# Kernel tuning notes

Measured on AMD Instinct MI355X. Metric: run time of the kernel, lower is better.

Reference implementation:

```python
import jax, jax.numpy as jnp
import numpy as np

N_PREV = 65536
BATCH = 2048
DIM = 128


def setup_inputs() -> dict:
    key = jax.random.key(0)
    k1, k2 = jax.random.split(key)
    n = N_PREV + BATCH
    target_lib = jax.random.normal(k1, (n, DIM), dtype=jnp.float32)
    reached_lib = jax.random.normal(k2, (n, DIM), dtype=jnp.float32)
    return {
        "target_goal_embedding_library": target_lib,
        "reached_goal_embedding_library": reached_lib,
        "batch_size": BATCH,
    }


def reference(target_goal_embedding_library, reached_goal_embedding_library, batch_size):
    # slice the library: last batch_size rows are current target/reached goals
    tg = target_goal_embedding_library[-batch_size:]      # [B, D]
    rg = reached_goal_embedding_library[-batch_size:]     # [B, D]
    prev = reached_goal_embedding_library[:-batch_size]   # [N_prev, D]

    # brute-force squared euclidean distances via gram trick: [B, N_prev]
    d2 = (
        jnp.sum(tg * tg, axis=-1, keepdims=True)
        - 2.0 * tg @ prev.T
        + jnp.sum(prev * prev, axis=-1)[None, :]
    )
    idx = jnp.argmin(d2, axis=1)          # top-1 nearest neighbor ids, [B]
    closest = prev[idx]                   # [B, D] gather

    # LP(g, s, r) = ||g - s|| - ||g - r||; value and grad wrt g, vmapped over batch
    def LP(g, s, r):
        return (
            jnp.sqrt(jnp.sum(jnp.square(g - s), axis=-1))
            - jnp.sqrt(jnp.sum(jnp.square(g - r), axis=-1))
        )

    IM_vals, IM_grads = jax.vmap(jax.value_and_grad(LP, 0), in_axes=(0, 0, 0))(
        tg, closest, rg
    )
    return IM_vals, IM_grads
```

## Files before the change

### kernel.cpp

```cpp
#include <hip/hip_runtime.h>
#include <math.h>

#define DIM 128
#define BATCH 2048
#define NPREV 65536
#define NCH 32
#define NJT 16
#define DELTA 0.4f

typedef __attribute__((ext_vector_type(8))) short bf16x8;
typedef __attribute__((ext_vector_type(4))) float f32x4;
typedef unsigned short u16;

static __device__ __forceinline__ unsigned short f2bf(float f) {
    unsigned int u = __float_as_uint(f);
    u += 0x7FFF + ((u >> 16) & 1);
    return (unsigned short)(u >> 16);
}

#define GLOAD16(g, l) __builtin_amdgcn_global_load_lds( \
    (const __attribute__((address_space(1))) void*)(g), \
    (__attribute__((address_space(3))) void*)(l), 16, 0, 0)

__global__ __launch_bounds__(256) void k_convB(const float* __restrict__ src,
                                               u16* __restrict__ dst,
                                               float* __restrict__ p2part) {
    int id = blockIdx.x * 256 + threadIdx.x;
    int img = id >> 10, c = id & 1023;
    int ks2 = c >> 9, rem = c & 511, row = rem >> 2, slot = rem & 3;
    int koct = slot ^ ((row >> 1) & 3);
    int srow = (img >> 1) * 128 + row;
    int scol = (img & 1) * 64 + ks2 * 32 + koct * 8;
    const float* s = src + (size_t)srow * DIM + scol;
    float4 f0 = *reinterpret_cast<const float4*>(s);
    float4 f1 = *reinterpret_cast<const float4*>(s + 4);
    float f[8] = {f0.x, f0.y, f0.z, f0.w, f1.x, f1.y, f1.z, f1.w};
    union { unsigned short us[8]; uint4 v; } o;
    float sum = 0.f;
    #pragma unroll
    for (int e = 0; e < 8; ++e) { o.us[e] = f2bf(f[e]); sum += f[e] * f[e]; }
    *reinterpret_cast<uint4*>(dst + (size_t)id * 8) = o.v;
    p2part[srow * 16 + (scol >> 3)] = sum;
}

__global__ __launch_bounds__(256) void k_prev2r(const float* __restrict__ p2part,
                                                float* __restrict__ prev2) {
    int row = blockIdx.x * 256 + threadIdx.x;
    const float4* p = reinterpret_cast<const float4*>(p2part + (size_t)row * 16);
    float4 a = p[0], b = p[1], c = p[2], d = p[3];
    float s = ((a.x + a.y) + (a.z + a.w)) + ((b.x + b.y) + (b.z + b.w))
            + ((c.x + c.y) + (c.z + c.w)) + ((d.x + d.y) + (d.z + d.w));
    prev2[row] = s;
}

__global__ __launch_bounds__(256) void k_convA(const float* __restrict__ src,
                                               u16* __restrict__ dst) {
    int id = blockIdx.x * 256 + threadIdx.x;
    int img = id >> 11, c = id & 2047;
    int ks2 = c >> 10, rem = c & 1023, row = rem >> 2, koct = rem & 3;
    int srow = (img >> 1) * 256 + row;
    int scol = (img & 1) * 64 + ks2 * 32 + koct * 8;
    const float* s = src + (size_t)srow * DIM + scol;
    float4 f0 = *reinterpret_cast<const float4*>(s);
    float4 f1 = *reinterpret_cast<const float4*>(s + 4);
    float f[8] = {f0.x, f0.y, f0.z, f0.w, f1.x, f1.y, f1.z, f1.w};
    union { unsigned short us[8]; uint4 v; } o;
    #pragma unroll
    for (int e = 0; e < 8; ++e) o.us[e] = f2bf(f[e]);
    *reinterpret_cast<uint4*>(dst + (size_t)id * 8) = o.v;
}

__global__ __launch_bounds__(512, 2) void k_gemm_argmin(
    const u16* __restrict__ Aimg, const u16* __restrict__ Bimg,
    const float* __restrict__ prev2, float4* __restrict__ partial)
{
    __shared__ __align__(16) u16 Bt[2][16384];

    const int t = threadIdx.x;
    const int lane = t & 63;
    const int w = t >> 6;
    const int l15 = lane & 15;
    const int lhi = lane >> 4;

    const int bid = blockIdx.x;
    const int mtile = bid >> 5;
    const int chunk = (bid & 7) + ((bid >> 3) & 3) * 8;

    const u16* gb0 = Bimg + (size_t)chunk * NJT * 16384;

    #pragma unroll
    for (int c = 0; c < 4; ++c)
        GLOAD16(gb0 + c * 4096 + t * 8, &Bt[0][c * 4096 + t * 8]);

    bf16x8 areg[2][2][2];
    {
        const u16* ab = Aimg + (size_t)mtile * 2 * 16384;
        #pragma unroll
        for (int kt = 0; kt < 2; ++kt)
            #pragma unroll
            for (int ks2 = 0; ks2 < 2; ++ks2)
                #pragma unroll
                for (int fm = 0; fm < 2; ++fm) {
                    int row = w * 32 + fm * 16 + l15;
                    areg[kt][ks2][fm] = *reinterpret_cast<const bf16x8*>(
                        ab + (size_t)kt * 16384 + (ks2 * 1024 + row * 4 + lhi) * 8);
                }
    }

    const int bbase = l15 * 64 + ((lhi ^ ((l15 >> 1) & 3)) << 4);
    const f32x4 z4 = {0.f, 0.f, 0.f, 0.f};

    float v1[2][4], v2[2][4]; int j1_[2][4], j2_[2][4];
    #pragma unroll
    for (int fm = 0; fm < 2; ++fm)
        #pragma unroll
        for (int r = 0; r < 4; ++r) {
            v1[fm][r] = INFINITY; v2[fm][r] = INFINITY;
            j1_[fm][r] = 0x7fffffff; j2_[fm][r] = 0x7fffffff;
        }

    for (int jt = 0; jt < NJT; ++jt) {
        const int p = jt & 1;
        __syncthreads();
        if (jt + 1 < NJT) {
            const u16* gb = gb0 + (size_t)(jt + 1) * 16384;
            u16* lb = Bt[p ^ 1];
            #pragma unroll
            for (int c = 0; c < 4; ++c)
                GLOAD16(gb + c * 4096 + t * 8, lb + c * 4096 + t * 8);
        }
        float p2f[8];
        #pragma unroll
        for (int fn = 0; fn < 8; ++fn)
            p2f[fn] = prev2[chunk * 2048 + jt * 128 + fn * 16 + l15];

        f32x4 acc[2][8];
        const char* Bc = (const char*)Bt[p];
        #pragma unroll
        for (int s = 0; s < 4; ++s) {
            const int img = s >> 1, ks2 = s & 1;
            bf16x8 bf[8];
            #pragma unroll
            for (int fn = 0; fn < 8; ++fn)
                bf[fn] = *reinterpret_cast<const bf16x8*>(
                    Bc + img * 16384 + ks2 * 8192 + fn * 1024 + bbase);
            if (s == 0) {
                #pragma unroll
                for (int fm = 0; fm < 2; ++fm)
                    #pragma unroll
                    for (int fn = 0; fn < 8; ++fn)
                        acc[fm][fn] = __builtin_amdgcn_mfma_f32_16x16x32_bf16(
                            areg[0][0][fm], bf[fn], z4, 0, 0, 0);
            } else {
                #pragma unroll
                for (int fm = 0; fm < 2; ++fm)
                    #pragma unroll
                    for (int fn = 0; fn < 8; ++fn)
                        acc[fm][fn] = __builtin_amdgcn_mfma_f32_16x16x32_bf16(
                            areg[img][ks2][fm], bf[fn], acc[fm][fn], 0, 0, 0);
            }
        }

        const int jb = chunk * 2048 + jt * 128 + l15;
        #pragma unroll
        for (int fm = 0; fm < 2; ++fm) {
            #pragma unroll
            for (int r = 0; r < 4; ++r) {
                float dmin = p2f[0] - 2.f * acc[fm][0][r]; int fs = 0;
                #pragma unroll
                for (int fn = 1; fn < 8; ++fn) {
                    float d = p2f[fn] - 2.f * acc[fm][fn][r];
                    if (d < dmin) { dmin = d; fs = fn; }
                }
                const int j = jb + fs * 16;
                const bool c1 = dmin < v1[fm][r];
                const bool c2 = dmin < v2[fm][r];
                v2[fm][r] = c1 ? v1[fm][r] : (c2 ? dmin : v2[fm][r]);
                j2_[fm][r] = c1 ? j1_[fm][r] : (c2 ? j    : j2_[fm][r]);
                v1[fm][r] = c1 ? dmin : v1[fm][r];
                j1_[fm][r] = c1 ? j    : j1_[fm][r];
            }
        }
    }

    #pragma unroll
    for (int fm = 0; fm < 2; ++fm) {
        #pragma unroll
        for (int r = 0; r < 4; ++r) {
            float a1 = v1[fm][r], a2 = v2[fm][r];
            int   b1 = j1_[fm][r], b2 = j2_[fm][r];
            #pragma unroll
            for (int m = 1; m < 16; m <<= 1) {
                float o1 = __shfl_xor(a1, m); int p1 = __shfl_xor(b1, m);
                float o2 = __shfl_xor(a2, m); int p2 = __shfl_xor(b2, m);
                bool a = (o1 < a1) || (o1 == a1 && p1 < b1);
                float c1v = a ? a1 : o1; int c1j = a ? b1 : p1;
                float c2v = a ? o2 : a2; int c2j = a ? p2 : b2;
                float w1  = a ? o1 : a1; int k1  = a ? p1 : b1;
                bool b = (c1v < c2v) || (c1v == c2v && c1j < c2j);
                a1 = w1; b1 = k1;
                a2 = b ? c1v : c2v; b2 = b ? c1j : c2j;
            }
            if (l15 == 0) {
                int row = w * 32 + fm * 16 + lhi * 4 + r;
                partial[(size_t)(mtile * 256 + row) * NCH + chunk] =
                    make_float4(a1, __int_as_float(b1), a2, __int_as_float(b2));
            }
        }
    }
}

__global__ __launch_bounds__(256) void k_final2(
    const float* __restrict__ tg, const float* __restrict__ rg,
    const float* __restrict__ prev, const float2* __restrict__ partial2,
    float* __restrict__ out_vals, float* __restrict__ out_grads)
{
    const int wv = threadIdx.x >> 6, lane = threadIdx.x & 63;
    const int i = blockIdx.x * 4 + wv;
    const float2 e = partial2[(size_t)i * 64 + lane];
    const float v = e.x; const int j = __float_as_int(e.y);

    float bv = v; int bj = j;
    #pragma unroll
    for (int m = 1; m < 64; m <<= 1) {
        float ov = __shfl_xor(bv, m); int oj = __shfl_xor(bj, m);
        if (ov < bv || (ov == bv && oj < bj)) { bv = ov; bj = oj; }
    }

    unsigned long long mask = __ballot(v <= bv + DELTA);
    const float2 g = *reinterpret_cast<const float2*>(tg + (size_t)i * DIM + 2 * lane);

    float bestd = INFINITY; int bestj = 0x7fffffff;
    while (mask) {
        int src = __ffsll(mask) - 1; mask &= mask - 1;
        int cj = __shfl(j, src);
        const float2 p = *reinterpret_cast<const float2*>(prev + (size_t)cj * DIM + 2 * lane);
        float dx = g.x - p.x, dy = g.y - p.y;
        float d = dx * dx + dy * dy;
        #pragma unroll
        for (int m = 1; m < 64; m <<= 1) d += __shfl_xor(d, m);
        if (d < bestd || (d == bestd && cj < bestj)) { bestd = d; bestj = cj; }
    }

    const float2 s = *reinterpret_cast<const float2*>(prev + (size_t)bestj * DIM + 2 * lane);
    const float2 r = *reinterpret_cast<const float2*>(rg + (size_t)i * DIM + 2 * lane);
    const float dsx = g.x - s.x, dsy = g.y - s.y;
    const float drx = g.x - r.x, dry = g.y - r.y;
    float ds = dsx * dsx + dsy * dsy;
    float dr = drx * drx + dry * dry;
    #pragma unroll
    for (int m = 1; m < 64; m <<= 1) { ds += __shfl_xor(ds, m); dr += __shfl_xor(dr, m); }
    const float sds = sqrtf(ds), sdr = sqrtf(dr);
    if (lane == 0) out_vals[i] = sds - sdr;
    const float is = 1.0f / sds, ir = 1.0f / sdr;
    float2 gr;
    gr.x = dsx * is - drx * ir;
    gr.y = dsy * is - dry * ir;
    *reinterpret_cast<float2*>(out_grads + (size_t)i * DIM + 2 * lane) = gr;
}

#define TM 128
#define TN 128
#define FNCHUNK 16
#define JT_PER_CHUNK 32

__global__ __launch_bounds__(256) void k_prev2(const float* __restrict__ prev,
                                               float* __restrict__ prev2,
                                               int nprev) {
    const int wave = threadIdx.x >> 6;
    const int lane = threadIdx.x & 63;
    const int row = blockIdx.x * 4 + wave;
    if (row >= nprev) return;
    const float2 v = *reinterpret_cast<const float2*>(prev + (size_t)row * DIM + 2 * lane);
    float s = v.x * v.x + v.y * v.y;
    #pragma unroll
    for (int m = 1; m < 64; m <<= 1) s += __shfl_xor(s, m);
    if (lane == 0) prev2[row] = s;
}

__global__ __launch_bounds__(256, 1) void k_argmin_fb(
    const float* __restrict__ tg, const float* __restrict__ prev,
    const float* __restrict__ prev2, float2* __restrict__ partial)
{
    __shared__ float4 tgL[TM * 32];
    __shared__ float4 pvL[TN * 32];
    __shared__ float  p2L[TN];
    const int t = threadIdx.x;
    const int rowTile = blockIdx.x;
    const int chunk = blockIdx.y;
    const float4* tgG = reinterpret_cast<const float4*>(tg + (size_t)rowTile * TM * DIM);
    #pragma unroll
    for (int i = 0; i < 16; ++i) {
        const int idx = t + 256 * i;
        const int row = idx >> 5, kk = idx & 31;
        tgL[row * 32 + (kk ^ (row & 7))] = tgG[idx];
    }
    const int tx = t & 15, ty = t >> 4;
    const int sa = ty & 7, sb = tx & 7;
    float minval[8]; int minidx[8];
    #pragma unroll
    for (int ri = 0; ri < 8; ++ri) { minval[ri] = INFINITY; minidx[ri] = 0x7fffffff; }
    const int jchunk0 = chunk * (JT_PER_CHUNK * TN);
    for (int jt = 0; jt < JT_PER_CHUNK; ++jt) {
        const int j0 = jchunk0 + jt * TN;
        __syncthreads();
        const float4* pvG = reinterpret_cast<const float4*>(prev + (size_t)j0 * DIM);
        #pragma unroll
        for (int i = 0; i < 16; ++i) {
            const int idx = t + 256 * i;
            const int row = idx >> 5, kk = idx & 31;
            pvL[row * 32 + (kk ^ (row & 7))] = pvG[idx];
        }
        if (t < TN) p2L[t] = prev2[j0 + t];
        __syncthreads();
        float acc[8][8];
        #pragma unroll
        for (int ri = 0; ri < 8; ++ri)
            #pragma unroll
            for (int ci = 0; ci < 8; ++ci) acc[ri][ci] = 0.f;
        #pragma unroll 2
        for (int kk = 0; kk < 32; ++kk) {
            float4 a[8], b[8];
            const int ka = kk ^ sa, kb = kk ^ sb;
            #pragma unroll
            for (int ri = 0; ri < 8; ++ri) a[ri] = tgL[(ty + 16 * ri) * 32 + ka];
            #pragma unroll
            for (int ci = 0; ci < 8; ++ci) b[ci] = pvL[(tx + 16 * ci) * 32 + kb];
            #pragma unroll
            for (int ri = 0; ri < 8; ++ri)
                #pragma unroll
                for (int ci = 0; ci < 8; ++ci) {
                    acc[ri][ci] += a[ri].x * b[ci].x;
                    acc[ri][ci] += a[ri].y * b[ci].y;
                    acc[ri][ci] += a[ri].z * b[ci].z;
                    acc[ri][ci] += a[ri].w * b[ci].w;
                }
        }
        #pragma unroll
        for (int ci = 0; ci < 8; ++ci) {
            const int jl = tx + 16 * ci;
            const int jg = j0 + jl;
            const float pj = p2L[jl];
            #pragma unroll
            for (int ri = 0; ri < 8; ++ri) {
                const float d = pj - 2.f * acc[ri][ci];
                if (d < minval[ri]) { minval[ri] = d; minidx[ri] = jg; }
            }
        }
    }
    __syncthreads();
    float2* red = reinterpret_cast<float2*>(pvL);
    #pragma unroll
    for (int ri = 0; ri < 8; ++ri) {
        const int row = ty + 16 * ri;
        red[row * 16 + tx] = make_float2(minval[ri], __int_as_float(minidx[ri]));
    }
    __syncthreads();
    if (t < TM) {
        float bv = INFINITY; int bi = 0x7fffffff;
        #pragma unroll
        for (int e = 0; e < 16; ++e) {
            const float2 p = red[t * 16 + e];
            const int pi = __float_as_int(p.y);
            if (p.x < bv || (p.x == bv && pi < bi)) { bv = p.x; bi = pi; }
        }
        partial[(size_t)(rowTile * TM + t) * FNCHUNK + chunk] =
            make_float2(bv, __int_as_float(bi));
    }
}

__global__ __launch_bounds__(256) void k_final_fb(
    const float* __restrict__ tg, const float* __restrict__ rg,
    const float* __restrict__ prev, const float2* __restrict__ partial,
    float* __restrict__ out_vals, float* __restrict__ out_grads)
{
    const int wave = threadIdx.x >> 6, lane = threadIdx.x & 63;
    const int i = blockIdx.x * 4 + wave;
    float bv = INFINITY; int bi = 0x7fffffff;
    if (lane < FNCHUNK) {
        const float2 p = partial[(size_t)i * FNCHUNK + lane];
        bv = p.x; bi = __float_as_int(p.y);
    }
    #pragma unroll
    for (int m = 1; m < 16; m <<= 1) {
        const float ov = __shfl_xor(bv, m);
        const int   oi = __shfl_xor(bi, m);
        if (ov < bv || (ov == bv && oi < bi)) { bv = ov; bi = oi; }
    }
    bi = __shfl(bi, 0);
    const float2 g = *reinterpret_cast<const float2*>(tg   + (size_t)i  * DIM + 2 * lane);
    const float2 s = *reinterpret_cast<const float2*>(prev + (size_t)bi * DIM + 2 * lane);
    const float2 r = *reinterpret_cast<const float2*>(rg   + (size_t)i  * DIM + 2 * lane);
    const float dsx = g.x - s.x, dsy = g.y - s.y;
    const float drx = g.x - r.x, dry = g.y - r.y;
    float ds = dsx * dsx + dsy * dsy;
    float dr = drx * drx + dry * dry;
    #pragma unroll
    for (int m = 1; m < 64; m <<= 1) { ds += __shfl_xor(ds, m); dr += __shfl_xor(dr, m); }
    const float sds = sqrtf(ds), sdr = sqrtf(dr);
    if (lane == 0) out_vals[i] = sds - sdr;
    const float is = 1.0f / sds, ir = 1.0f / sdr;
    float2 gr;
    gr.x = dsx * is - drx * ir;
    gr.y = dsy * is - dry * ir;
    *reinterpret_cast<float2*>(out_grads + (size_t)i * DIM + 2 * lane) = gr;
}

extern "C" void kernel_launch(void* const* d_in, const int* in_sizes, int n_in,
                              void* d_out, int out_size, void* d_ws, size_t ws_size,
                              hipStream_t stream) {
    const float* target  = (const float*)d_in[0];
    const float* reached = (const float*)d_in[1];
    const int n_total = in_sizes[0] / DIM;
    const int nprev = n_total - BATCH;

    const float* tg   = target  + (size_t)nprev * DIM;
    const float* rg   = reached + (size_t)nprev * DIM;
    const float* prev = reached;

    float* out_vals  = (float*)d_out;
    float* out_grads = out_vals + BATCH;

    const size_t offB  = 0;
    const size_t offA  = (size_t)1024 * 8192 * 2;
    const size_t offP2 = offA + (size_t)16 * 16384 * 2;
    const size_t offPP = offP2 + (size_t)NPREV * 4;
    const size_t offPt = offPP + (size_t)NPREV * 16 * 4;
    const size_t need  = offPt + (size_t)BATCH * NCH * sizeof(float4);

    if (nprev == NPREV && ws_size >= need) {
        u16*    Bb      = (u16*)((char*)d_ws + offB);
        u16*    Ab      = (u16*)((char*)d_ws + offA);
        float*  prev2   = (float*)((char*)d_ws + offP2);
        float*  p2part  = (float*)((char*)d_ws + offPP);
        float4* partial = (float4*)((char*)d_ws + offPt);

        k_convB<<<(1024 * 1024) / 256, 256, 0, stream>>>(prev, Bb, p2part);
        k_convA<<<(16 * 2048) / 256, 256, 0, stream>>>(tg, Ab);
        k_prev2r<<<NPREV / 256, 256, 0, stream>>>(p2part, prev2);
        k_gemm_argmin<<<256, 512, 0, stream>>>(Ab, Bb, prev2, partial);
        k_final2<<<BATCH / 4, 256, 0, stream>>>(tg, rg, prev, (const float2*)partial,
                                                out_vals, out_grads);
    } else {
        float*  prev2   = (float*)d_ws;
        float2* partial = (float2*)((char*)d_ws + (size_t)nprev * sizeof(float));
        k_prev2<<<nprev / 4, 256, 0, stream>>>(prev, prev2, nprev);
        dim3 grid(BATCH / TM, FNCHUNK);
        k_argmin_fb<<<grid, 256, 0, stream>>>(tg, prev, prev2, partial);
        k_final_fb<<<BATCH / 4, 256, 0, stream>>>(tg, rg, prev, partial, out_vals, out_grads);
    }
}
```

Measured before the change: 67.62 us.

## Pack column index into float key bits and re-tile GEMM warps 4x4

```diff
diff --git a/kernel.cpp b/kernel.cpp
--- a/kernel.cpp
+++ b/kernel.cpp
@@ -6,7 +6,7 @@
 #define NPREV 65536
 #define NCH 32
 #define NJT 16
-#define DELTA 0.4f
+#define DELTA 0.8f
 
 typedef __attribute__((ext_vector_type(8))) short bf16x8;
 typedef __attribute__((ext_vector_type(4))) float f32x4;
@@ -44,13 +44,13 @@
 }
 
 __global__ __launch_bounds__(256) void k_prev2r(const float* __restrict__ p2part,
-                                                float* __restrict__ prev2) {
+                                                float* __restrict__ p2h) {
     int row = blockIdx.x * 256 + threadIdx.x;
     const float4* p = reinterpret_cast<const float4*>(p2part + (size_t)row * 16);
     float4 a = p[0], b = p[1], c = p[2], d = p[3];
     float s = ((a.x + a.y) + (a.z + a.w)) + ((b.x + b.y) + (b.z + b.w))
             + ((c.x + c.y) + (c.z + c.w)) + ((d.x + d.y) + (d.z + d.w));
-    prev2[row] = s;
+    p2h[row] = -0.5f * s;
 }
 
 __global__ __launch_bounds__(256) void k_convA(const float* __restrict__ src,
@@ -72,13 +72,15 @@
 
 __global__ __launch_bounds__(512, 2) void k_gemm_argmin(
     const u16* __restrict__ Aimg, const u16* __restrict__ Bimg,
-    const float* __restrict__ prev2, float4* __restrict__ partial)
+    const float* __restrict__ p2h, float4* __restrict__ partial)
 {
     __shared__ __align__(16) u16 Bt[2][16384];
 
     const int t = threadIdx.x;
     const int lane = t & 63;
     const int w = t >> 6;
+    const int wrow = w & 3;
+    const int cg = w >> 2;
     const int l15 = lane & 15;
     const int lhi = lane >> 4;
 
@@ -92,32 +94,35 @@
     for (int c = 0; c < 4; ++c)
         GLOAD16(gb0 + c * 4096 + t * 8, &Bt[0][c * 4096 + t * 8]);
 
-    bf16x8 areg[2][2][2];
+    bf16x8 areg[4][4];
     {
         const u16* ab = Aimg + (size_t)mtile * 2 * 16384;
         #pragma unroll
-        for (int kt = 0; kt < 2; ++kt)
-            #pragma unroll
-            for (int ks2 = 0; ks2 < 2; ++ks2)
-                #pragma unroll
-                for (int fm = 0; fm < 2; ++fm) {
-                    int row = w * 32 + fm * 16 + l15;
-                    areg[kt][ks2][fm] = *reinterpret_cast<const bf16x8*>(
-                        ab + (size_t)kt * 16384 + (ks2 * 1024 + row * 4 + lhi) * 8);
-                }
-    }
-
-    const int bbase = l15 * 64 + ((lhi ^ ((l15 >> 1) & 3)) << 4);
-    const f32x4 z4 = {0.f, 0.f, 0.f, 0.f};
-
-    float v1[2][4], v2[2][4]; int j1_[2][4], j2_[2][4];
-    #pragma unroll
-    for (int fm = 0; fm < 2; ++fm)
-        #pragma unroll
-        for (int r = 0; r < 4; ++r) {
-            v1[fm][r] = INFINITY; v2[fm][r] = INFINITY;
-            j1_[fm][r] = 0x7fffffff; j2_[fm][r] = 0x7fffffff;
-        }
+        for (int s = 0; s < 4; ++s) {
+            const int img = s >> 1, ks2 = s & 1;
+            #pragma unroll
+            for (int fm = 0; fm < 4; ++fm) {
+                int row = wrow * 64 + fm * 16 + l15;
+                areg[s][fm] = *reinterpret_cast<const bf16x8*>(
+                    ab + (size_t)img * 16384 + (ks2 * 1024 + row * 4 + lhi) * 8);
+            }
+        }
+    }
+
+    const int sbyte = (lhi ^ ((l15 >> 1) & 3)) << 4;
+    const int bbase = (cg * 64 + l15) * 64 + sbyte;
+    const unsigned sbase = ((unsigned)cg << 10) | ((unsigned)l15 << 2);
+    const int phbase = chunk * 2048 + cg * 64 + l15;
+
+    float v1[4][4], v2[4][4];
+    #pragma unroll
+    for (int fm = 0; fm < 4; ++fm)
+        #pragma unroll
+        for (int r = 0; r < 4; ++r) { v1[fm][r] = -INFINITY; v2[fm][r] = -INFINITY; }
+
+    float phc[4];
+    #pragma unroll
+    for (int fn = 0; fn < 4; ++fn) phc[fn] = p2h[phbase + fn * 16];
 
     for (int jt = 0; jt < NJT; ++jt) {
         const int p = jt & 1;
@@ -129,84 +134,95 @@
             for (int c = 0; c < 4; ++c)
                 GLOAD16(gb + c * 4096 + t * 8, lb + c * 4096 + t * 8);
         }
-        float p2f[8];
-        #pragma unroll
-        for (int fn = 0; fn < 8; ++fn)
-            p2f[fn] = prev2[chunk * 2048 + jt * 128 + fn * 16 + l15];
-
-        f32x4 acc[2][8];
+        float phn[4];
+        if (jt + 1 < NJT) {
+            #pragma unroll
+            for (int fn = 0; fn < 4; ++fn)
+                phn[fn] = p2h[phbase + (jt + 1) * 128 + fn * 16];
+        }
+
+        f32x4 acc[4][4];
+        #pragma unroll
+        for (int fn = 0; fn < 4; ++fn) {
+            const float pv = phc[fn];
+            #pragma unroll
+            for (int fm = 0; fm < 4; ++fm)
+                acc[fm][fn] = (f32x4){pv, pv, pv, pv};
+        }
+
         const char* Bc = (const char*)Bt[p];
         #pragma unroll
         for (int s = 0; s < 4; ++s) {
             const int img = s >> 1, ks2 = s & 1;
-            bf16x8 bf[8];
-            #pragma unroll
-            for (int fn = 0; fn < 8; ++fn)
+            bf16x8 bf[4];
+            #pragma unroll
+            for (int fn = 0; fn < 4; ++fn)
                 bf[fn] = *reinterpret_cast<const bf16x8*>(
                     Bc + img * 16384 + ks2 * 8192 + fn * 1024 + bbase);
-            if (s == 0) {
+            #pragma unroll
+            for (int fm = 0; fm < 4; ++fm)
                 #pragma unroll
-                for (int fm = 0; fm < 2; ++fm)
-                    #pragma unroll
-                    for (int fn = 0; fn < 8; ++fn)
-                        acc[fm][fn] = __builtin_amdgcn_mfma_f32_16x16x32_bf16(
-                            areg[0][0][fm], bf[fn], z4, 0, 0, 0);
-            } else {
-                #pragma unroll
-                for (int fm = 0; fm < 2; ++fm)
-                    #pragma unroll
-                    for (int fn = 0; fn < 8; ++fn)
-                        acc[fm][fn] = __builtin_amdgcn_mfma_f32_16x16x32_bf16(
-                            areg[img][ks2][fm], bf[fn], acc[fm][fn], 0, 0, 0);
+                for (int fn = 0; fn < 4; ++fn)
+                    acc[fm][fn] = __builtin_amdgcn_mfma_f32_16x16x32_bf16(
+                        areg[s][fm], bf[fn], acc[fm][fn], 0, 0, 0);
+        }
+
+        const unsigned stampv = sbase | ((unsigned)jt << 6);
+        #pragma unroll
+        for (int fm = 0; fm < 4; ++fm) {
+            #pragma unroll
+            for (int r = 0; r < 4; ++r) {
+                unsigned u0 = (__float_as_uint(acc[fm][0][r]) & ~0x7FFu);
+                unsigned u1 = (__float_as_uint(acc[fm][1][r]) & ~0x7FFu) | 1u;
+                unsigned u2 = (__float_as_uint(acc[fm][2][r]) & ~0x7FFu) | 2u;
+                unsigned u3 = (__float_as_uint(acc[fm][3][r]) & ~0x7FFu) | 3u;
+                float m = fmaxf(fmaxf(__uint_as_float(u0), __uint_as_float(u1)),
+                                fmaxf(__uint_as_float(u2), __uint_as_float(u3)));
+                float key = __uint_as_float(__float_as_uint(m) | stampv);
+                float tm = fminf(v1[fm][r], key);
+                v1[fm][r] = fmaxf(v1[fm][r], key);
+                v2[fm][r] = fmaxf(v2[fm][r], tm);
             }
         }
 
-        const int jb = chunk * 2048 + jt * 128 + l15;
-        #pragma unroll
-        for (int fm = 0; fm < 2; ++fm) {
-            #pragma unroll
-            for (int r = 0; r < 4; ++r) {
-                float dmin = p2f[0] - 2.f * acc[fm][0][r]; int fs = 0;
-                #pragma unroll
-                for (int fn = 1; fn < 8; ++fn) {
-                    float d = p2f[fn] - 2.f * acc[fm][fn][r];
-                    if (d < dmin) { dmin = d; fs = fn; }
-                }
-                const int j = jb + fs * 16;
-                const bool c1 = dmin < v1[fm][r];
-                const bool c2 = dmin < v2[fm][r];
-                v2[fm][r] = c1 ? v1[fm][r] : (c2 ? dmin : v2[fm][r]);
-                j2_[fm][r] = c1 ? j1_[fm][r] : (c2 ? j    : j2_[fm][r]);
-                v1[fm][r] = c1 ? dmin : v1[fm][r];
-                j1_[fm][r] = c1 ? j    : j1_[fm][r];
-            }
-        }
-    }
-
-    #pragma unroll
-    for (int fm = 0; fm < 2; ++fm) {
+        if (jt + 1 < NJT) {
+            #pragma unroll
+            for (int fn = 0; fn < 4; ++fn) phc[fn] = phn[fn];
+        }
+    }
+
+    float2* red = reinterpret_cast<float2*>(Bt);
+    #pragma unroll
+    for (int fm = 0; fm < 4; ++fm) {
         #pragma unroll
         for (int r = 0; r < 4; ++r) {
             float a1 = v1[fm][r], a2 = v2[fm][r];
-            int   b1 = j1_[fm][r], b2 = j2_[fm][r];
             #pragma unroll
             for (int m = 1; m < 16; m <<= 1) {
-                float o1 = __shfl_xor(a1, m); int p1 = __shfl_xor(b1, m);
-                float o2 = __shfl_xor(a2, m); int p2 = __shfl_xor(b2, m);
-                bool a = (o1 < a1) || (o1 == a1 && p1 < b1);
-                float c1v = a ? a1 : o1; int c1j = a ? b1 : p1;
-                float c2v = a ? o2 : a2; int c2j = a ? p2 : b2;
-                float w1  = a ? o1 : a1; int k1  = a ? p1 : b1;
-                bool b = (c1v < c2v) || (c1v == c2v && c1j < c2j);
-                a1 = w1; b1 = k1;
-                a2 = b ? c1v : c2v; b2 = b ? c1j : c2j;
+                float o1 = __shfl_xor(a1, m), o2 = __shfl_xor(a2, m);
+                float n2 = fmaxf(fminf(a1, o1), fmaxf(a2, o2));
+                a1 = fmaxf(a1, o1); a2 = n2;
             }
             if (l15 == 0) {
-                int row = w * 32 + fm * 16 + lhi * 4 + r;
-                partial[(size_t)(mtile * 256 + row) * NCH + chunk] =
-                    make_float4(a1, __int_as_float(b1), a2, __int_as_float(b2));
+                int row = wrow * 64 + fm * 16 + lhi * 4 + r;
+                red[row * 2 + cg] = make_float2(a1, a2);
             }
         }
+    }
+    __syncthreads();
+    if (t < 256) {
+        float2 x = red[t * 2 + 0], y = red[t * 2 + 1];
+        float u1f = fmaxf(x.x, y.x);
+        float u2f = fmaxf(fminf(x.x, y.x), fmaxf(x.y, y.y));
+        unsigned ua = __float_as_uint(u1f), ub = __float_as_uint(u2f);
+        int ja = chunk * 2048 + (int)((ua >> 6) & 15) * 128 + (int)((ua >> 10) & 1) * 64
+               + (int)(ua & 3) * 16 + (int)((ua >> 2) & 15);
+        int jb = chunk * 2048 + (int)((ub >> 6) & 15) * 128 + (int)((ub >> 10) & 1) * 64
+               + (int)(ub & 3) * 16 + (int)((ub >> 2) & 15);
+        float d1 = -2.0f * __uint_as_float(ua & ~0x7FFu);
+        float d2 = -2.0f * __uint_as_float(ub & ~0x7FFu);
+        partial[(size_t)(mtile * 256 + t) * NCH + chunk] =
+            make_float4(d1, __int_as_float(ja), d2, __int_as_float(jb));
     }
 }
 
@@ -431,14 +447,14 @@
     if (nprev == NPREV && ws_size >= need) {
         u16*    Bb      = (u16*)((char*)d_ws + offB);
         u16*    Ab      = (u16*)((char*)d_ws + offA);
-        float*  prev2   = (float*)((char*)d_ws + offP2);
+        float*  p2h     = (float*)((char*)d_ws + offP2);
         float*  p2part  = (float*)((char*)d_ws + offPP);
         float4* partial = (float4*)((char*)d_ws + offPt);
 
         k_convB<<<(1024 * 1024) / 256, 256, 0, stream>>>(prev, Bb, p2part);
         k_convA<<<(16 * 2048) / 256, 256, 0, stream>>>(tg, Ab);
-        k_prev2r<<<NPREV / 256, 256, 0, stream>>>(p2part, prev2);
-        k_gemm_argmin<<<256, 512, 0, stream>>>(Ab, Bb, prev2, partial);
+        k_prev2r<<<NPREV / 256, 256, 0, stream>>>(p2part, p2h);
+        k_gemm_argmin<<<256, 512, 0, stream>>>(Ab, Bb, p2h, partial);
         k_final2<<<BATCH / 4, 256, 0, stream>>>(tg, rg, prev, (const float2*)partial,
                                                 out_vals, out_grads);
     } else {
```

Result: faster. 61.13 us (-9.6%).
